# Performance work log

Hardware: AMD Instinct MI355X
Metric: run time of the kernel (lower is better)

Reference implementation:

```python
import jax, jax.numpy as jnp
import numpy as np

NUM_CLASSES = 21
THRESH = 0.5
NEGPOS = 3
VAR0, VAR1 = 0.1, 0.2
FEAT = 19
N_ANCH = 9
B = 256
NUM_OBJS = 12
P = FEAT * FEAT * N_ANCH  # 3249


def make_priors():
    # 19x19 grid, 3 scales x 3 aspect ratios (1, 2, 1/2) -> 9 anchors/cell, center form
    cxy = (np.arange(FEAT, dtype=np.float32) + 0.5) / FEAT
    cx, cy = np.meshgrid(cxy, cxy, indexing='ij')  # [19,19]
    scales = np.array([0.1, 0.2, 0.35], dtype=np.float32)
    ratios = np.array([1.0, 2.0, 0.5], dtype=np.float32)
    w = (scales[:, None] * np.sqrt(ratios)[None, :]).reshape(-1)  # [9]
    h = (scales[:, None] / np.sqrt(ratios)[None, :]).reshape(-1)
    cx = np.broadcast_to(cx[:, :, None], (FEAT, FEAT, N_ANCH))
    cy = np.broadcast_to(cy[:, :, None], (FEAT, FEAT, N_ANCH))
    w = np.broadcast_to(w[None, None, :], (FEAT, FEAT, N_ANCH))
    h = np.broadcast_to(h[None, None, :], (FEAT, FEAT, N_ANCH))
    pri = np.stack([cx, cy, w, h], axis=-1).reshape(-1, 4)
    return jnp.asarray(np.clip(pri, 1e-3, 1.0))


def setup_inputs() -> dict:
    key = jax.random.key(0)
    k1, k2, k3, k4, k5 = jax.random.split(key, 5)
    loc_data = jax.random.normal(k1, (B, P, 4), dtype=jnp.float32)
    conf_data = jax.random.normal(k2, (B, P, NUM_CLASSES), dtype=jnp.float32)
    priors = make_priors()
    xy = jax.random.uniform(k3, (B, NUM_OBJS, 2), minval=0.05, maxval=0.65)
    wh = jax.random.uniform(k4, (B, NUM_OBJS, 2), minval=0.05, maxval=0.30)
    labels = jax.random.randint(k5, (B, NUM_OBJS), 0, NUM_CLASSES - 1).astype(jnp.float32)
    targets = jnp.concatenate([xy, xy + wh, labels[..., None]], axis=-1)  # [B,O,5]
    return {"loc_data": loc_data, "conf_data": conf_data, "priors": priors, "targets": targets}


def point_form(boxes):  # (cx,cy,w,h) -> (x1,y1,x2,y2)
    return jnp.concatenate([boxes[:, :2] - boxes[:, 2:] / 2,
                            boxes[:, :2] + boxes[:, 2:] / 2], axis=1)


def jaccard(a, b):  # a: [n,4], b: [m,4] point form -> [n,m]
    lt = jnp.maximum(a[:, None, :2], b[None, :, :2])
    rb = jnp.minimum(a[:, None, 2:], b[None, :, 2:])
    inter = jnp.prod(jnp.clip(rb - lt, 0.0, None), axis=-1)
    area_a = jnp.prod(a[:, 2:] - a[:, :2], axis=-1)
    area_b = jnp.prod(b[:, 2:] - b[:, :2], axis=-1)
    return inter / (area_a[:, None] + area_b[None, :] - inter)


def encode(matched, priors):  # matched point-form [P,4], priors center-form [P,4]
    g_cxcy = ((matched[:, :2] + matched[:, 2:]) / 2 - priors[:, :2]) / (VAR0 * priors[:, 2:])
    g_wh = jnp.log((matched[:, 2:] - matched[:, :2]) / priors[:, 2:]) / VAR1
    return jnp.concatenate([g_cxcy, g_wh], axis=1)


def match_one(truths, labels, priors, priors_pt):
    overlaps = jaccard(truths, priors_pt)          # [O,P]
    best_prior_idx = jnp.argmax(overlaps, axis=1)  # [O]
    best_truth_ov = jnp.max(overlaps, axis=0)      # [P]
    best_truth_idx = jnp.argmax(overlaps, axis=0)  # [P]
    best_truth_ov = best_truth_ov.at[best_prior_idx].set(2.0)
    best_truth_idx = best_truth_idx.at[best_prior_idx].set(jnp.arange(truths.shape[0]))
    matches = truths[best_truth_idx]               # [P,4]
    conf = labels[best_truth_idx] + 1
    conf = jnp.where(best_truth_ov < THRESH, 0, conf)
    return encode(matches, priors), conf


def reference(loc_data, conf_data, priors, targets):
    truths = targets[:, :, :4]
    labels = targets[:, :, 4].astype(jnp.int32)
    priors_pt = point_form(priors)
    loc_t, conf_t = jax.vmap(lambda t, l: match_one(t, l, priors, priors_pt))(truths, labels)
    loc_t = jax.lax.stop_gradient(loc_t)
    conf_t = jax.lax.stop_gradient(conf_t)

    pos = conf_t > 0                                               # [B,P]
    # smooth L1 (sum) over matched priors
    d = loc_data - loc_t
    ad = jnp.abs(d)
    sl1 = jnp.where(ad < 1.0, 0.5 * d * d, ad - 0.5)
    loss_l = jnp.sum(sl1 * pos[..., None].astype(sl1.dtype))

    # per-prior CE = logsumexp - logit[target]
    lse = jax.nn.logsumexp(conf_data, axis=-1)                     # [B,P]
    gathered = jnp.take_along_axis(conf_data, conf_t[..., None], axis=2)[..., 0]
    ce = lse - gathered                                            # [B,P]

    # hard negative mining: double argsort rank of neg losses
    loss_c_mine = jnp.where(pos, 0.0, ce)
    loss_idx = jnp.argsort(-loss_c_mine, axis=1)
    idx_rank = jnp.argsort(loss_idx, axis=1)
    num_pos = jnp.sum(pos, axis=1, keepdims=True)                  # [B,1]
    num_neg = jnp.minimum(NEGPOS * num_pos, P - 1)
    neg = idx_rank < num_neg

    sel = pos | neg
    loss_c = jnp.sum(jnp.where(sel, ce, 0.0))

    have_centerloss = jnp.max(sel.reshape(B, FEAT, FEAT, N_ANCH), axis=3).reshape(-1)
    conf_t_featuremap = jnp.max(conf_t.reshape(B, FEAT, FEAT, N_ANCH), axis=3).reshape(-1)

    N = jnp.sum(num_pos).astype(loc_data.dtype)
    return loss_l / N, loss_c / N, conf_t_featuremap, have_centerloss
```

## Files before the change

### kernel.cpp

```cpp
#include <hip/hip_runtime.h>
#include <math.h>

#pragma clang fp contract(off)

#define BB      256
#define PP      3249
#define NCLS    21
#define NOBJ    12
#define CELLS   361
#define THRESH_ 0.5f

typedef float vf4 __attribute__((ext_vector_type(4), aligned(4)));


__global__ __launch_bounds__(1024, 4) void fused_kernel(
    const float* __restrict__ loc, const float* __restrict__ conf,
    const float* __restrict__ priors, const float* __restrict__ targets,
    int* __restrict__ numpos, double* __restrict__ lossl,
    double* __restrict__ lossc, float* __restrict__ out)
{
    const int b = blockIdx.x, tid = threadIdx.x;
    const int lane = tid & 63, wid = tid >> 6;

    __shared__ float s_tx1[NOBJ], s_ty1[NOBJ], s_tx2[NOBJ], s_ty2[NOBJ];
    __shared__ float s_area_t[NOBJ];
    __shared__ int   s_label[NOBJ];
    __shared__ float s_bov[PP];
    __shared__ short s_bidx[PP];
    __shared__ int   s_bpi[NOBJ];
    __shared__ float s_wov[NOBJ][16];
    __shared__ int   s_widx[NOBJ][16];
    __shared__ unsigned long long s_key[PP];
    __shared__ unsigned char s_ct[PP];
    __shared__ unsigned char s_sel[PP];
    __shared__ int s_hist[256];
    __shared__ int s_chosen, s_knext, s_nneg;
    __shared__ double s_pl[16];
    __shared__ int    s_pn[16];
    __shared__ double s_pc[16];

    if (tid < NOBJ) {
        const float* t = targets + ((size_t)b * NOBJ + tid) * 5;
        float x1 = t[0], y1 = t[1], x2 = t[2], y2 = t[3];
        s_tx1[tid] = x1; s_ty1[tid] = y1; s_tx2[tid] = x2; s_ty2[tid] = y2;
        s_label[tid] = (int)t[4];
        s_area_t[tid] = (x2 - x1) * (y2 - y1);
    }
    __syncthreads();

    const float* confb = conf + (size_t)b * PP * NCLS;
    vf4 q[5]; float q20 = 0.0f;
    {
        const vf4* cd4 = (const vf4*)(confb + (size_t)tid * NCLS);
#pragma unroll
        for (int v = 0; v < 5; ++v) q[v] = cd4[v];
        q20 = confb[(size_t)tid * NCLS + 20];
    }

    float l_bov[NOBJ];
    int   l_bidx[NOBJ];
#pragma unroll
    for (int j = 0; j < NOBJ; ++j) { l_bov[j] = -1.0f; l_bidx[j] = 0x7FFFFFFF; }

    for (int p = tid; p < PP; p += 1024) {
        float cx = priors[4*p+0], cy = priors[4*p+1], w = priors[4*p+2], h = priors[4*p+3];
        float px1 = cx - w / 2.0f, py1 = cy - h / 2.0f;
        float px2 = cx + w / 2.0f, py2 = cy + h / 2.0f;
        float area_p = (px2 - px1) * (py2 - py1);
        float bov = -1.0f; int bidx = 0;
#pragma unroll
        for (int j = 0; j < NOBJ; ++j) {
            float ltx = fmaxf(s_tx1[j], px1);
            float lty = fmaxf(s_ty1[j], py1);
            float rbx = fminf(s_tx2[j], px2);
            float rby = fminf(s_ty2[j], py2);
            float iw = fmaxf(rbx - ltx, 0.0f);
            float ih = fmaxf(rby - lty, 0.0f);
            float inter = iw * ih;
            float iou = inter / ((s_area_t[j] + area_p) - inter);
            if (iou > bov) { bov = iou; bidx = j; }
            if (iou > l_bov[j]) { l_bov[j] = iou; l_bidx[j] = p; }
        }
        s_bov[p] = bov;
        s_bidx[p] = (short)bidx;
    }

#pragma unroll
    for (int j = 0; j < NOBJ; ++j) {
        float ov = l_bov[j]; int ix = l_bidx[j];
#pragma unroll
        for (int off = 32; off > 0; off >>= 1) {
            float ov2 = __shfl_xor(ov, off);
            int   ix2 = __shfl_xor(ix, off);
            if (ov2 > ov || (ov2 == ov && ix2 < ix)) { ov = ov2; ix = ix2; }
        }
        if (lane == 0) { s_wov[j][wid] = ov; s_widx[j][wid] = ix; }
    }
    __syncthreads();
    if (tid < NOBJ) {
        float ov = s_wov[tid][0]; int ix = s_widx[tid][0];
#pragma unroll
        for (int w2 = 1; w2 < 16; ++w2) {
            float ov2 = s_wov[tid][w2]; int ix2 = s_widx[tid][w2];
            if (ov2 > ov || (ov2 == ov && ix2 < ix)) { ov = ov2; ix = ix2; }
        }
        s_bpi[tid] = ix;
    }
    __syncthreads();

    int bpi[NOBJ];
#pragma unroll
    for (int j = 0; j < NOBJ; ++j) bpi[j] = s_bpi[j];

    int my_pos = 0;
    double my_lossl = 0.0;
    for (int p = tid; p < PP; p += 1024) {
        const int pn = p + 1024;
        vf4 qn[5]; float qn20 = 0.0f;
        if (pn < PP) {
            const vf4* cd4n = (const vf4*)(confb + (size_t)pn * NCLS);
#pragma unroll
            for (int v = 0; v < 5; ++v) qn[v] = cd4n[v];
            qn20 = confb[(size_t)pn * NCLS + 20];
        }

        int jov = -1;
#pragma unroll
        for (int j = 0; j < NOBJ; ++j) if (bpi[j] == p) jov = j;
        int idx; float ov;
        if (jov >= 0) { idx = jov; ov = 2.0f; }
        else          { idx = (int)s_bidx[p]; ov = s_bov[p]; }
        int c = (ov < THRESH_) ? 0 : (s_label[idx] + 1);
        s_ct[p] = (unsigned char)c;

        float rw[NCLS];
#pragma unroll
        for (int v = 0; v < 5; ++v) {
            rw[4*v+0] = q[v][0]; rw[4*v+1] = q[v][1]; rw[4*v+2] = q[v][2]; rw[4*v+3] = q[v][3];
        }
        rw[20] = q20;

        float m = rw[0];
#pragma unroll
        for (int k = 1; k < NCLS; ++k) m = fmaxf(m, rw[k]);
        float s = 0.0f;
#pragma unroll
        for (int k = 0; k < NCLS; ++k) s += expf(rw[k] - m);
        float cdc = rw[0];
#pragma unroll
        for (int k = 1; k < NCLS; ++k) if (c == k) cdc = rw[k];
        float ce = (logf(s) + m) - cdc;

        float v = (c > 0) ? 0.0f : ce;
        s_key[p] = ((unsigned long long)__float_as_uint(v) << 32)
                 | (unsigned int)(0xFFFFFFFFu - (unsigned int)p);
        s_bov[p] = ce;

        if (c > 0) {
            ++my_pos;
            float cx = priors[4*p+0], cy = priors[4*p+1], w = priors[4*p+2], h = priors[4*p+3];
            float m0 = s_tx1[idx], m1 = s_ty1[idx], m2 = s_tx2[idx], m3 = s_ty2[idx];
            float g0 = ((m0 + m2) / 2.0f - cx) / (0.1f * w);
            float g1 = ((m1 + m3) / 2.0f - cy) / (0.1f * h);
            float g2 = logf((m2 - m0) / w) / 0.2f;
            float g3 = logf((m3 - m1) / h) / 0.2f;
            const float* ld = loc + ((size_t)b * PP + p) * 4;
            float d0 = ld[0] - g0, d1 = ld[1] - g1, d2 = ld[2] - g2, d3 = ld[3] - g3;
            float a0 = fabsf(d0), a1 = fabsf(d1), a2 = fabsf(d2), a3 = fabsf(d3);
            my_lossl += (double)((a0 < 1.0f) ? 0.5f * d0 * d0 : a0 - 0.5f);
            my_lossl += (double)((a1 < 1.0f) ? 0.5f * d1 * d1 : a1 - 0.5f);
            my_lossl += (double)((a2 < 1.0f) ? 0.5f * d2 * d2 : a2 - 0.5f);
            my_lossl += (double)((a3 < 1.0f) ? 0.5f * d3 * d3 : a3 - 0.5f);
        }

#pragma unroll
        for (int v2 = 0; v2 < 5; ++v2) q[v2] = qn[v2];
        q20 = qn20;
    }
#pragma unroll
    for (int off = 32; off > 0; off >>= 1) {
        my_lossl += __shfl_down(my_lossl, off);
        my_pos   += __shfl_down(my_pos, off);
    }
    if (lane == 0) { s_pl[wid] = my_lossl; s_pn[wid] = my_pos; }
    __syncthreads();
    if (tid == 0) {
        double L = 0.0; int n = 0;
#pragma unroll
        for (int w2 = 0; w2 < 16; ++w2) { L += s_pl[w2]; n += s_pn[w2]; }
        lossl[b] = L; numpos[b] = n;
        s_nneg = min(3 * n, PP - 1);
    }
    __syncthreads();

    const int ds[6] = {56, 48, 40, 32, 8, 0};
    unsigned long long prefix = 0ull, pmask = 0ull;
    int kk = s_nneg;
#pragma unroll
    for (int ri = 0; ri < 6; ++ri) {
        const int d = ds[ri];
        if (tid < 256) s_hist[tid] = 0;
        __syncthreads();
        for (int i = tid; i < PP; i += 1024) {
            unsigned long long key = s_key[i];
            if ((key & pmask) == prefix)
                atomicAdd(&s_hist[(int)((key >> d) & 0xFF)], 1);
        }
        __syncthreads();
        if (tid < 64) {
            int h0 = s_hist[4*lane+0], h1 = s_hist[4*lane+1];
            int h2 = s_hist[4*lane+2], h3 = s_hist[4*lane+3];
            int ls = h0 + h1 + h2 + h3;
            int x = ls;
#pragma unroll
            for (int off = 1; off < 64; off <<= 1) {
                int y = __shfl_down(x, off);
                if (lane + off < 64) x += y;
            }
            int excl = x - ls;
            int cb3 = excl;
            int cb2 = cb3 + h3;
            int cb1 = cb2 + h2;
            int cb0 = cb1 + h1;
            if (cb3 < kk && kk <= cb3 + h3) { s_chosen = 4*lane+3; s_knext = kk - cb3; }
            if (cb2 < kk && kk <= cb2 + h2) { s_chosen = 4*lane+2; s_knext = kk - cb2; }
            if (cb1 < kk && kk <= cb1 + h1) { s_chosen = 4*lane+1; s_knext = kk - cb1; }
            if (cb0 < kk && kk <= cb0 + h0) { s_chosen = 4*lane+0; s_knext = kk - cb0; }
        }
        __syncthreads();
        prefix |= ((unsigned long long)(unsigned int)s_chosen) << d;
        pmask  |= 0xFFull << d;
        kk = s_knext;
        if (d == 32) { prefix |= 0xFFFF0000ull; pmask |= 0xFFFF0000ull; }
        __syncthreads();
    }
    const unsigned long long kth = prefix;

    double my_c = 0.0;
    for (int p = tid; p < PP; p += 1024) {
        int c = s_ct[p];
        bool sel = (c > 0) || (s_key[p] >= kth);
        s_sel[p] = sel ? 1 : 0;
        if (sel) my_c += (double)s_bov[p];
    }
    __syncthreads();

    for (int cI = tid; cI < CELLS; cI += 1024) {
        int mc = 0, hv = 0;
#pragma unroll
        for (int a = 0; a < 9; ++a) {
            int p = cI * 9 + a;
            int cv = s_ct[p];
            mc = (cv > mc) ? cv : mc;
            hv |= s_sel[p];
        }
        out[2 + (size_t)b * CELLS + cI] = (float)mc;
        out[2 + (size_t)BB * CELLS + (size_t)b * CELLS + cI] = (float)hv;
    }

#pragma unroll
    for (int off = 32; off > 0; off >>= 1) my_c += __shfl_down(my_c, off);
    if (lane == 0) s_pc[wid] = my_c;
    __syncthreads();
    if (tid == 0) {
        double L = 0.0;
#pragma unroll
        for (int w2 = 0; w2 < 16; ++w2) L += s_pc[w2];
        lossc[b] = L;
    }
}

__global__ __launch_bounds__(256) void finalize_kernel(
    const int* __restrict__ numpos, const double* __restrict__ lossl,
    const double* __restrict__ lossc, float* __restrict__ out)
{
    __shared__ double s_l[256], s_c[256];
    __shared__ int s_n[256];
    int tid = threadIdx.x;
    s_n[tid] = numpos[tid];
    s_l[tid] = lossl[tid];
    s_c[tid] = lossc[tid];
    __syncthreads();
    for (int s = 128; s > 0; s >>= 1) {
        if (tid < s) { s_n[tid] += s_n[tid + s]; s_l[tid] += s_l[tid + s]; s_c[tid] += s_c[tid + s]; }
        __syncthreads();
    }
    if (tid == 0) {
        double N = (double)s_n[0];
        out[0] = (float)(s_l[0] / N);
        out[1] = (float)(s_c[0] / N);
    }
}

extern "C" void kernel_launch(void* const* d_in, const int* in_sizes, int n_in,
                              void* d_out, int out_size, void* d_ws, size_t ws_size,
                              hipStream_t stream) {
    const float* loc     = (const float*)d_in[0];
    const float* conf    = (const float*)d_in[1];
    const float* priors  = (const float*)d_in[2];
    const float* targets = (const float*)d_in[3];
    float* out = (float*)d_out;

    double* ws_lossl  = (double*)d_ws;
    double* ws_lossc  = ws_lossl + BB;
    int*    ws_numpos = (int*)(ws_lossc + BB);

    hipLaunchKernelGGL(fused_kernel, dim3(BB), dim3(1024), 0, stream,
                       loc, conf, priors, targets, ws_numpos, ws_lossl, ws_lossc, out);
    hipLaunchKernelGGL(finalize_kernel, dim3(1), dim3(256), 0, stream,
                       ws_numpos, ws_lossl, ws_lossc, out);
}
```

Baseline: 143.2 us.

## Split fused loss kernel into chunked parallel stage and per-batch selection stage

The single per-batch kernel (256 blocks of 1024 threads) becomes two kernels. The first spreads IoU matching and logsumexp over 13 chunks per batch row with 256-thread blocks, and writes keys, lse, match info and per-chunk best-prior partials to workspace. The second gathers these into shared memory, applies the forced best-prior matches, then runs the radix select and the loss sums. The aim is more parallelism and occupancy for the conf-bandwidth-heavy stage, at the cost of extra global round trips for keys and lse, an extra launch, and re-reading conf for positive targets.

```diff
diff --git a/kernel.cpp b/kernel.cpp
--- a/kernel.cpp
+++ b/kernel.cpp
@@ -9,35 +9,28 @@
 #define NOBJ    12
 #define CELLS   361
 #define THRESH_ 0.5f
+#define NCHUNK  13
 
 typedef float vf4 __attribute__((ext_vector_type(4), aligned(4)));
-
-
-__global__ __launch_bounds__(1024, 4) void fused_kernel(
-    const float* __restrict__ loc, const float* __restrict__ conf,
-    const float* __restrict__ priors, const float* __restrict__ targets,
-    int* __restrict__ numpos, double* __restrict__ lossl,
-    double* __restrict__ lossc, float* __restrict__ out)
+typedef unsigned long long u64;
+typedef unsigned int u32;
+typedef unsigned char u8;
+
+
+__global__ __launch_bounds__(256, 8) void k1_heavy(
+    const float* __restrict__ conf, const float* __restrict__ priors,
+    const float* __restrict__ targets,
+    float* __restrict__ g_lse, u64* __restrict__ g_key,
+    u8* __restrict__ g_mi, u64* __restrict__ g_part)
 {
-    const int b = blockIdx.x, tid = threadIdx.x;
-    const int lane = tid & 63, wid = tid >> 6;
-
-    __shared__ float s_tx1[NOBJ], s_ty1[NOBJ], s_tx2[NOBJ], s_ty2[NOBJ];
-    __shared__ float s_area_t[NOBJ];
+    const int b = blockIdx.y, chunk = blockIdx.x;
+    const int tid = threadIdx.x, lane = tid & 63, wv = tid >> 6;
+    const int p = chunk * 256 + tid;
+    const bool valid = (p < PP);
+
+    __shared__ float s_tx1[NOBJ], s_ty1[NOBJ], s_tx2[NOBJ], s_ty2[NOBJ], s_area_t[NOBJ];
     __shared__ int   s_label[NOBJ];
-    __shared__ float s_bov[PP];
-    __shared__ short s_bidx[PP];
-    __shared__ int   s_bpi[NOBJ];
-    __shared__ float s_wov[NOBJ][16];
-    __shared__ int   s_widx[NOBJ][16];
-    __shared__ unsigned long long s_key[PP];
-    __shared__ unsigned char s_ct[PP];
-    __shared__ unsigned char s_sel[PP];
-    __shared__ int s_hist[256];
-    __shared__ int s_chosen, s_knext, s_nneg;
-    __shared__ double s_pl[16];
-    __shared__ int    s_pn[16];
-    __shared__ double s_pc[16];
+    __shared__ u64   s_part[4][NOBJ];
 
     if (tid < NOBJ) {
         const float* t = targets + ((size_t)b * NOBJ + tid) * 5;
@@ -48,26 +41,13 @@
     }
     __syncthreads();
 
-    const float* confb = conf + (size_t)b * PP * NCLS;
-    vf4 q[5]; float q20 = 0.0f;
-    {
-        const vf4* cd4 = (const vf4*)(confb + (size_t)tid * NCLS);
-#pragma unroll
-        for (int v = 0; v < 5; ++v) q[v] = cd4[v];
-        q20 = confb[(size_t)tid * NCLS + 20];
-    }
-
-    float l_bov[NOBJ];
-    int   l_bidx[NOBJ];
-#pragma unroll
-    for (int j = 0; j < NOBJ; ++j) { l_bov[j] = -1.0f; l_bidx[j] = 0x7FFFFFFF; }
-
-    for (int p = tid; p < PP; p += 1024) {
-        float cx = priors[4*p+0], cy = priors[4*p+1], w = priors[4*p+2], h = priors[4*p+3];
-        float px1 = cx - w / 2.0f, py1 = cy - h / 2.0f;
-        float px2 = cx + w / 2.0f, py2 = cy + h / 2.0f;
+    float iou_j[NOBJ];
+    float bov = -1.0f; int bidx = 0;
+    if (valid) {
+        float4 pw = ((const float4*)priors)[p];
+        float px1 = pw.x - pw.z / 2.0f, py1 = pw.y - pw.w / 2.0f;
+        float px2 = pw.x + pw.z / 2.0f, py2 = pw.y + pw.w / 2.0f;
         float area_p = (px2 - px1) * (py2 - py1);
-        float bov = -1.0f; int bidx = 0;
 #pragma unroll
         for (int j = 0; j < NOBJ; ++j) {
             float ltx = fmaxf(s_tx1[j], px1);
@@ -78,111 +58,162 @@
             float ih = fmaxf(rby - lty, 0.0f);
             float inter = iw * ih;
             float iou = inter / ((s_area_t[j] + area_p) - inter);
+            iou_j[j] = iou;
             if (iou > bov) { bov = iou; bidx = j; }
-            if (iou > l_bov[j]) { l_bov[j] = iou; l_bidx[j] = p; }
-        }
-        s_bov[p] = bov;
-        s_bidx[p] = (short)bidx;
+        }
+    } else {
+#pragma unroll
+        for (int j = 0; j < NOBJ; ++j) iou_j[j] = -1.0f;
+    }
+
+    const float* confb = conf + (size_t)b * PP * NCLS;
+    vf4 q[5]; float q20 = 0.0f;
+    if (valid) {
+        const vf4* cd4 = (const vf4*)(confb + (size_t)p * NCLS);
+#pragma unroll
+        for (int v = 0; v < 5; ++v) q[v] = cd4[v];
+        q20 = confb[(size_t)p * NCLS + 20];
     }
 
 #pragma unroll
     for (int j = 0; j < NOBJ; ++j) {
-        float ov = l_bov[j]; int ix = l_bidx[j];
+        u64 k = valid ? (((u64)__float_as_uint(iou_j[j]) << 32)
+                         | (u32)(0xFFFFFFFFu - (u32)p))
+                      : 0ull;
 #pragma unroll
         for (int off = 32; off > 0; off >>= 1) {
-            float ov2 = __shfl_xor(ov, off);
-            int   ix2 = __shfl_xor(ix, off);
-            if (ov2 > ov || (ov2 == ov && ix2 < ix)) { ov = ov2; ix = ix2; }
-        }
-        if (lane == 0) { s_wov[j][wid] = ov; s_widx[j][wid] = ix; }
+            u64 o = __shfl_xor(k, off);
+            if (o > k) k = o;
+        }
+        if (lane == 0) s_part[wv][j] = k;
     }
     __syncthreads();
     if (tid < NOBJ) {
-        float ov = s_wov[tid][0]; int ix = s_widx[tid][0];
-#pragma unroll
-        for (int w2 = 1; w2 < 16; ++w2) {
-            float ov2 = s_wov[tid][w2]; int ix2 = s_widx[tid][w2];
-            if (ov2 > ov || (ov2 == ov && ix2 < ix)) { ov = ov2; ix = ix2; }
-        }
-        s_bpi[tid] = ix;
-    }
-    __syncthreads();
-
-    int bpi[NOBJ];
-#pragma unroll
-    for (int j = 0; j < NOBJ; ++j) bpi[j] = s_bpi[j];
+        u64 m = s_part[0][tid];
+#pragma unroll
+        for (int w = 1; w < 4; ++w) { u64 o = s_part[w][tid]; if (o > m) m = o; }
+        g_part[((size_t)b * NCHUNK + chunk) * NOBJ + tid] = m;
+    }
+
+    if (!valid) return;
+
+    int c = (bov < THRESH_) ? 0 : (s_label[bidx] + 1);
+    g_mi[(size_t)b * PP + p] = (u8)(((bov < THRESH_) ? 0 : 0x80) | bidx);
+
+    float rw[NCLS];
+#pragma unroll
+    for (int v = 0; v < 5; ++v) {
+        rw[4*v+0] = q[v][0]; rw[4*v+1] = q[v][1]; rw[4*v+2] = q[v][2]; rw[4*v+3] = q[v][3];
+    }
+    rw[20] = q20;
+    float m = rw[0];
+#pragma unroll
+    for (int k = 1; k < NCLS; ++k) m = fmaxf(m, rw[k]);
+    float s = 0.0f;
+#pragma unroll
+    for (int k = 0; k < NCLS; ++k) s += expf(rw[k] - m);
+    float lse = logf(s) + m;
+    float cdc = rw[0];
+#pragma unroll
+    for (int k = 1; k < NCLS; ++k) if (c == k) cdc = rw[k];
+    float ce = lse - cdc;
+
+    g_lse[(size_t)b * PP + p] = lse;
+    float v = (c > 0) ? 0.0f : ce;
+    g_key[(size_t)b * PP + p] = ((u64)__float_as_uint(v) << 32)
+                              | (u32)(0xFFFFFFFFu - (u32)p);
+}
+
+__global__ __launch_bounds__(1024) void k2_select(
+    const float* __restrict__ conf, const float* __restrict__ loc,
+    const float* __restrict__ priors, const float* __restrict__ targets,
+    const float* __restrict__ g_lse, const u64* __restrict__ g_key,
+    const u8* __restrict__ g_mi, const u64* __restrict__ g_part,
+    int* __restrict__ numpos, double* __restrict__ lossl,
+    double* __restrict__ lossc, float* __restrict__ out)
+{
+    const int b = blockIdx.x, tid = threadIdx.x;
+    const int lane = tid & 63, wid = tid >> 6;
+
+    __shared__ u64 s_key[PP];
+    __shared__ u8  s_mi[PP];
+    __shared__ u8  s_ct[PP];
+    __shared__ u8  s_sel[PP];
+    __shared__ int s_hist[256];
+    __shared__ float s_tx1[NOBJ], s_ty1[NOBJ], s_tx2[NOBJ], s_ty2[NOBJ];
+    __shared__ int   s_label[NOBJ], s_bpi[NOBJ];
+    __shared__ int s_chosen, s_knext, s_nneg;
+    __shared__ double s_pl[16], s_pc[16];
+    __shared__ int    s_pn[16];
+
+    if (tid < NOBJ) {
+        const float* t = targets + ((size_t)b * NOBJ + tid) * 5;
+        s_tx1[tid] = t[0]; s_ty1[tid] = t[1]; s_tx2[tid] = t[2]; s_ty2[tid] = t[3];
+        s_label[tid] = (int)t[4];
+        u64 m = 0ull;
+#pragma unroll
+        for (int c2 = 0; c2 < NCHUNK; ++c2) {
+            u64 o = g_part[((size_t)b * NCHUNK + c2) * NOBJ + tid];
+            if (o > m) m = o;
+        }
+        s_bpi[tid] = (int)(0xFFFFFFFFu - (u32)(m & 0xFFFFFFFFull));
+    }
+    __syncthreads();
+
+    const size_t bo = (size_t)b * PP;
+    for (int p = tid; p < PP; p += 1024) {
+        s_key[p] = g_key[bo + p];
+        u8 mi = g_mi[bo + p];
+        s_mi[p] = mi;
+        s_ct[p] = (u8)((mi & 0x80) ? (s_label[mi & 15] + 1) : 0);
+    }
+    __syncthreads();
+
+    if (tid == 0) {
+        for (int j = 0; j < NOBJ; ++j) {
+            int p = s_bpi[j];
+            s_ct[p] = (u8)(s_label[j] + 1);
+            s_key[p] = (u64)(u32)(0xFFFFFFFFu - (u32)p);
+        }
+    }
+    __syncthreads();
 
     int my_pos = 0;
-    double my_lossl = 0.0;
+    double my_lossl = 0.0, my_c = 0.0;
     for (int p = tid; p < PP; p += 1024) {
-        const int pn = p + 1024;
-        vf4 qn[5]; float qn20 = 0.0f;
-        if (pn < PP) {
-            const vf4* cd4n = (const vf4*)(confb + (size_t)pn * NCLS);
-#pragma unroll
-            for (int v = 0; v < 5; ++v) qn[v] = cd4n[v];
-            qn20 = confb[(size_t)pn * NCLS + 20];
-        }
-
-        int jov = -1;
-#pragma unroll
-        for (int j = 0; j < NOBJ; ++j) if (bpi[j] == p) jov = j;
-        int idx; float ov;
-        if (jov >= 0) { idx = jov; ov = 2.0f; }
-        else          { idx = (int)s_bidx[p]; ov = s_bov[p]; }
-        int c = (ov < THRESH_) ? 0 : (s_label[idx] + 1);
-        s_ct[p] = (unsigned char)c;
-
-        float rw[NCLS];
-#pragma unroll
-        for (int v = 0; v < 5; ++v) {
-            rw[4*v+0] = q[v][0]; rw[4*v+1] = q[v][1]; rw[4*v+2] = q[v][2]; rw[4*v+3] = q[v][3];
-        }
-        rw[20] = q20;
-
-        float m = rw[0];
-#pragma unroll
-        for (int k = 1; k < NCLS; ++k) m = fmaxf(m, rw[k]);
-        float s = 0.0f;
-#pragma unroll
-        for (int k = 0; k < NCLS; ++k) s += expf(rw[k] - m);
-        float cdc = rw[0];
-#pragma unroll
-        for (int k = 1; k < NCLS; ++k) if (c == k) cdc = rw[k];
-        float ce = (logf(s) + m) - cdc;
-
-        float v = (c > 0) ? 0.0f : ce;
-        s_key[p] = ((unsigned long long)__float_as_uint(v) << 32)
-                 | (unsigned int)(0xFFFFFFFFu - (unsigned int)p);
-        s_bov[p] = ce;
-
+        int c = s_ct[p];
         if (c > 0) {
             ++my_pos;
-            float cx = priors[4*p+0], cy = priors[4*p+1], w = priors[4*p+2], h = priors[4*p+3];
+            int idx = -1;
+#pragma unroll
+            for (int j = 0; j < NOBJ; ++j) if (s_bpi[j] == p) idx = j;
+            if (idx < 0) idx = s_mi[p] & 15;
+            float cdc = conf[(bo + p) * NCLS + c];
+            my_c += (double)(g_lse[bo + p] - cdc);
+            float4 pw = ((const float4*)priors)[p];
             float m0 = s_tx1[idx], m1 = s_ty1[idx], m2 = s_tx2[idx], m3 = s_ty2[idx];
-            float g0 = ((m0 + m2) / 2.0f - cx) / (0.1f * w);
-            float g1 = ((m1 + m3) / 2.0f - cy) / (0.1f * h);
-            float g2 = logf((m2 - m0) / w) / 0.2f;
-            float g3 = logf((m3 - m1) / h) / 0.2f;
-            const float* ld = loc + ((size_t)b * PP + p) * 4;
-            float d0 = ld[0] - g0, d1 = ld[1] - g1, d2 = ld[2] - g2, d3 = ld[3] - g3;
+            float g0 = ((m0 + m2) / 2.0f - pw.x) / (0.1f * pw.z);
+            float g1 = ((m1 + m3) / 2.0f - pw.y) / (0.1f * pw.w);
+            float g2 = logf((m2 - m0) / pw.z) / 0.2f;
+            float g3 = logf((m3 - m1) / pw.w) / 0.2f;
+            float4 lw = ((const float4*)loc)[bo + p];
+            float d0 = lw.x - g0, d1 = lw.y - g1, d2 = lw.z - g2, d3 = lw.w - g3;
             float a0 = fabsf(d0), a1 = fabsf(d1), a2 = fabsf(d2), a3 = fabsf(d3);
             my_lossl += (double)((a0 < 1.0f) ? 0.5f * d0 * d0 : a0 - 0.5f);
             my_lossl += (double)((a1 < 1.0f) ? 0.5f * d1 * d1 : a1 - 0.5f);
             my_lossl += (double)((a2 < 1.0f) ? 0.5f * d2 * d2 : a2 - 0.5f);
             my_lossl += (double)((a3 < 1.0f) ? 0.5f * d3 * d3 : a3 - 0.5f);
         }
-
-#pragma unroll
-        for (int v2 = 0; v2 < 5; ++v2) q[v2] = qn[v2];
-        q20 = qn20;
-    }
-#pragma unroll
-    for (int off = 32; off > 0; off >>= 1) {
-        my_lossl += __shfl_down(my_lossl, off);
-        my_pos   += __shfl_down(my_pos, off);
-    }
-    if (lane == 0) { s_pl[wid] = my_lossl; s_pn[wid] = my_pos; }
+    }
+    {
+        double rl = my_lossl; int rp = my_pos;
+#pragma unroll
+        for (int off = 32; off > 0; off >>= 1) {
+            rl += __shfl_down(rl, off);
+            rp += __shfl_down(rp, off);
+        }
+        if (lane == 0) { s_pl[wid] = rl; s_pn[wid] = rp; }
+    }
     __syncthreads();
     if (tid == 0) {
         double L = 0.0; int n = 0;
@@ -194,7 +225,7 @@
     __syncthreads();
 
     const int ds[6] = {56, 48, 40, 32, 8, 0};
-    unsigned long long prefix = 0ull, pmask = 0ull;
+    u64 prefix = 0ull, pmask = 0ull;
     int kk = s_nneg;
 #pragma unroll
     for (int ri = 0; ri < 6; ++ri) {
@@ -202,7 +233,7 @@
         if (tid < 256) s_hist[tid] = 0;
         __syncthreads();
         for (int i = tid; i < PP; i += 1024) {
-            unsigned long long key = s_key[i];
+            u64 key = s_key[i];
             if ((key & pmask) == prefix)
                 atomicAdd(&s_hist[(int)((key >> d) & 0xFF)], 1);
         }
@@ -228,20 +259,21 @@
             if (cb0 < kk && kk <= cb0 + h0) { s_chosen = 4*lane+0; s_knext = kk - cb0; }
         }
         __syncthreads();
-        prefix |= ((unsigned long long)(unsigned int)s_chosen) << d;
+        prefix |= ((u64)(u32)s_chosen) << d;
         pmask  |= 0xFFull << d;
         kk = s_knext;
         if (d == 32) { prefix |= 0xFFFF0000ull; pmask |= 0xFFFF0000ull; }
         __syncthreads();
     }
-    const unsigned long long kth = prefix;
-
-    double my_c = 0.0;
+    const u64 kth = prefix;
+
     for (int p = tid; p < PP; p += 1024) {
         int c = s_ct[p];
-        bool sel = (c > 0) || (s_key[p] >= kth);
+        u64 key = s_key[p];
+        bool sel = (c > 0) || (key >= kth);
         s_sel[p] = sel ? 1 : 0;
-        if (sel) my_c += (double)s_bov[p];
+        if (sel && c == 0)
+            my_c += (double)__uint_as_float((u32)(key >> 32));
     }
     __syncthreads();
 
@@ -301,12 +333,19 @@
     const float* targets = (const float*)d_in[3];
     float* out = (float*)d_out;
 
-    double* ws_lossl  = (double*)d_ws;
-    double* ws_lossc  = ws_lossl + BB;
-    int*    ws_numpos = (int*)(ws_lossc + BB);
-
-    hipLaunchKernelGGL(fused_kernel, dim3(BB), dim3(1024), 0, stream,
-                       loc, conf, priors, targets, ws_numpos, ws_lossl, ws_lossc, out);
+    double* ws_lossl = (double*)d_ws;
+    double* ws_lossc = ws_lossl + BB;
+    u64*    ws_part  = (u64*)(ws_lossc + BB);
+    u64*    ws_key   = ws_part + (size_t)BB * NCHUNK * NOBJ;
+    float*  ws_lse   = (float*)(ws_key + (size_t)BB * PP);
+    int*    ws_numpos = (int*)(ws_lse + (size_t)BB * PP);
+    u8*     ws_mi    = (u8*)(ws_numpos + BB);
+
+    hipLaunchKernelGGL(k1_heavy, dim3(NCHUNK, BB), dim3(256), 0, stream,
+                       conf, priors, targets, ws_lse, ws_key, ws_mi, ws_part);
+    hipLaunchKernelGGL(k2_select, dim3(BB), dim3(1024), 0, stream,
+                       conf, loc, priors, targets, ws_lse, ws_key, ws_mi, ws_part,
+                       ws_numpos, ws_lossl, ws_lossc, out);
     hipLaunchKernelGGL(finalize_kernel, dim3(1), dim3(256), 0, stream,
                        ws_numpos, ws_lossl, ws_lossc, out);
 }
```

Measured after the change: 141.4 us. About the same (-1.2%).
